# Kernel tuning notes

Hardware: AMD Instinct MI355X
Metric: run time of the kernel (lower is better)

The kernel has to match this reference:

```python
import jax, jax.numpy as jnp
import numpy as np

B, NB, F, N = 8192, 64, 256, 1_000_000
K = 8            # per-channel top-k
KS = K // 2 + 1  # conv1d kernel size = 5
H, OUT = 256, 128
DN = ('NWC', 'WIO', 'NWC')


def setup_inputs() -> dict:
    key = jax.random.key(0)
    ks = jax.random.split(key, 7)
    return {
        'node_ids': jax.random.randint(ks[0], (B,), 0, N, dtype=jnp.int64) if jax.config.jax_enable_x64 else jax.random.randint(ks[0], (B,), 0, N, dtype=jnp.int32),
        'neighbors': jax.random.randint(ks[1], (B, NB), 0, N, dtype=jnp.int32),
        'feat_table': jax.random.normal(ks[2], (N, F), dtype=jnp.float32),
        'W1': jax.random.normal(ks[3], (KS, F, H), dtype=jnp.float32) * 0.05,
        'b1': jnp.zeros((H,), dtype=jnp.float32),
        'W2': jax.random.normal(ks[4], (KS, H, OUT), dtype=jnp.float32) * 0.05,
        'b2': jnp.zeros((OUT,), dtype=jnp.float32),
    }


def reference(node_ids, neighbors, feat_table, W1, b1, W2, b2):
    node_feats = feat_table[node_ids][:, None, :]          # [B, 1, F]
    nb_feats = feat_table[neighbors]                       # [B, NB, F] irregular gather
    # per-channel top-k over neighbors
    topk, _ = jax.lax.top_k(jnp.transpose(nb_feats, (0, 2, 1)), K)  # [B, F, K]
    topk = jnp.transpose(topk, (0, 2, 1))                  # [B, K, F]
    x = jnp.concatenate([node_feats, topk], axis=1)        # [B, K+1, F]
    h = jax.lax.conv_general_dilated(x, W1, (1,), 'VALID', dimension_numbers=DN) + b1  # [B, K+2-KS, H]
    o = jax.lax.conv_general_dilated(h, W2, (1,), 'VALID', dimension_numbers=DN) + b2  # [B, 1, OUT]
    return o[:, 0, :]                                      # [B, OUT]
```

## Files before the change

### kernel.cpp

```cpp
#include <hip/hip_runtime.h>
#include <hip/hip_bf16.h>

namespace {
constexpr int kB    = 8192;
constexpr int kNB   = 64;
constexpr int kF    = 256;
constexpr int kK    = 8;
constexpr int kKS   = 5;
constexpr int kH    = 256;
constexpr int kOUT  = 128;
constexpr int kXR   = 9;
constexpr int kTO   = 5;
constexpr int kBM   = 16;

constexpr int XPAD = 258;
constexpr int HPAD = 1290;

constexpr size_t W1T_OFF = 0;
constexpr size_t W2T_OFF = W1T_OFF + (size_t)kKS * kH * kF * 2;

typedef __attribute__((ext_vector_type(8))) short short8;
typedef __attribute__((ext_vector_type(4))) float f32x4;
}

using bf16 = __hip_bfloat16;

__device__ __forceinline__ unsigned short f2bf(float f) {
  bf16 h = __float2bfloat16(f);
  return *reinterpret_cast<unsigned short*>(&h);
}

__global__ void convert_weights(const float* __restrict__ W1,
                                const float* __restrict__ W2,
                                bf16* __restrict__ w1t, bf16* __restrict__ w2t)
{
  const int i = blockIdx.x * 256 + threadIdx.x;
  const int stride = gridDim.x * 256;
  for (int idx = i; idx < kKS * kH * kF; idx += stride) {
    const int f  = idx & 255;
    const int hc = (idx >> 8) & 255;
    const int dt = idx >> 16;
    w1t[idx] = __float2bfloat16(W1[(dt * kF + f) * kH + hc]);
  }
  for (int idx = i; idx < kOUT * kKS * kH; idx += stride) {
    const int k = idx % (kKS * kH);
    const int o = idx / (kKS * kH);
    w2t[idx] = __float2bfloat16(W2[k * kOUT + o]);
  }
}

__global__ __launch_bounds__(256)
void fused_all(const int* __restrict__ node_ids,
               const int* __restrict__ neighbors,
               const float* __restrict__ feat,
               const bf16* __restrict__ w1t, const bf16* __restrict__ w2t,
               const float* __restrict__ b1, const float* __restrict__ b2,
               float* __restrict__ out)
{
  __shared__ bf16 smem[kBM * kXR * XPAD];
  bf16* xs = smem;
  bf16* hs = smem;

  const int tid  = threadIdx.x;
  const int wave = tid >> 6;
  const int lane = tid & 63;
  const int r = lane & 15;
  const int q = lane >> 4;
  const int bbase = blockIdx.x * kBM;
  const int f4 = lane << 2;

  for (int bb = 0; bb < 4; ++bb) {
    const int bl = wave * 4 + bb;
    const int b  = bbase + bl;
    const int myn = neighbors[(size_t)b * kNB + lane];
    const int nid = node_ids[b];
    const float4 nodev = *reinterpret_cast<const float4*>(feat + (size_t)nid * kF + f4);

    float tk[4][kK];
#pragma unroll
    for (int c = 0; c < 4; ++c)
#pragma unroll
      for (int k = 0; k < kK; ++k) tk[c][k] = -INFINITY;

    auto ce4 = [&](const float4& v) {
      const float vv[4] = {v.x, v.y, v.z, v.w};
#pragma unroll
      for (int c = 0; c < 4; ++c) {
        tk[c][kK - 1] = fmaxf(tk[c][kK - 1], vv[c]);
#pragma unroll
        for (int k = kK - 1; k > 0; --k) {
          const float hi = fmaxf(tk[c][k - 1], tk[c][k]);
          const float lo = fminf(tk[c][k - 1], tk[c][k]);
          tk[c][k - 1] = hi;
          tk[c][k]     = lo;
        }
      }
    };

    float4 buf[8];
#pragma unroll
    for (int i = 0; i < 8; ++i) {
      const int rr = __builtin_amdgcn_readlane(myn, i);
      buf[i] = *reinterpret_cast<const float4*>(feat + (size_t)rr * kF + f4);
    }
    for (int g = 1; g < 8; ++g) {
#pragma unroll
      for (int i = 0; i < 8; ++i) {
        const float4 v = buf[i];
        const int rr = __builtin_amdgcn_readlane(myn, g * 8 + i);
        buf[i] = *reinterpret_cast<const float4*>(feat + (size_t)rr * kF + f4);
        ce4(v);
      }
    }
#pragma unroll
    for (int i = 0; i < 8; ++i) ce4(buf[i]);

    bf16* xb = xs + (size_t)bl * kXR * XPAD + f4;
    {
      ushort4 s = {f2bf(nodev.x), f2bf(nodev.y), f2bf(nodev.z), f2bf(nodev.w)};
      *reinterpret_cast<ushort4*>(xb) = s;
    }
#pragma unroll
    for (int k = 0; k < kK; ++k) {
      ushort4 s = {f2bf(tk[0][k]), f2bf(tk[1][k]), f2bf(tk[2][k]), f2bf(tk[3][k])};
      *reinterpret_cast<ushort4*>(xb + (size_t)(1 + k) * XPAD) = s;
    }
  }
  __syncthreads();

  const int ntb = wave * 64;
  f32x4 acc[kTO][4];
#pragma unroll
  for (int n = 0; n < 4; ++n) {
    const float bv = b1[ntb + n * 16 + r];
#pragma unroll
    for (int m = 0; m < kTO; ++m) acc[m][n] = (f32x4){bv, bv, bv, bv};
  }

  for (int kk = 0; kk < 8; ++kk) {
    short8 a[kXR];
#pragma unroll
    for (int rr = 0; rr < kXR; ++rr)
      a[rr] = *reinterpret_cast<const short8*>(&xs[(r * kXR + rr) * XPAD + kk * 32 + q * 8]);
#pragma unroll
    for (int dt = 0; dt < kKS; ++dt) {
      short8 bfr[4];
#pragma unroll
      for (int n = 0; n < 4; ++n)
        bfr[n] = *reinterpret_cast<const short8*>(
            &w1t[((size_t)(dt * kH + ntb + n * 16 + r)) * kF + kk * 32 + q * 8]);
#pragma unroll
      for (int m = 0; m < kTO; ++m)
#pragma unroll
        for (int n = 0; n < 4; ++n)
          acc[m][n] = __builtin_amdgcn_mfma_f32_16x16x32_bf16(a[m + dt], bfr[n], acc[m][n], 0, 0, 0);
    }
  }
  __syncthreads();

#pragma unroll
  for (int m = 0; m < kTO; ++m)
#pragma unroll
    for (int n = 0; n < 4; ++n)
#pragma unroll
      for (int j = 0; j < 4; ++j)
        hs[(q * 4 + j) * HPAD + m * kH + ntb + n * 16 + r] = __float2bfloat16(acc[m][n][j]);
  __syncthreads();

  const int ob = wave * 32;
  f32x4 acc2[2];
#pragma unroll
  for (int n = 0; n < 2; ++n) {
    const float bv = b2[ob + n * 16 + r];
    acc2[n] = (f32x4){bv, bv, bv, bv};
  }
  for (int ks = 0; ks < 40; ++ks) {
    short8 a2 = *reinterpret_cast<const short8*>(&hs[r * HPAD + ks * 32 + q * 8]);
#pragma unroll
    for (int n = 0; n < 2; ++n) {
      short8 b2f = *reinterpret_cast<const short8*>(
          &w2t[(size_t)(ob + n * 16 + r) * (kKS * kH) + ks * 32 + q * 8]);
      acc2[n] = __builtin_amdgcn_mfma_f32_16x16x32_bf16(a2, b2f, acc2[n], 0, 0, 0);
    }
  }
#pragma unroll
  for (int n = 0; n < 2; ++n)
#pragma unroll
    for (int j = 0; j < 4; ++j)
      out[(size_t)(bbase + q * 4 + j) * kOUT + ob + n * 16 + r] = acc2[n][j];
}

extern "C" void kernel_launch(void* const* d_in, const int* in_sizes, int n_in,
                              void* d_out, int out_size, void* d_ws, size_t ws_size,
                              hipStream_t stream) {
  const int*   node_ids  = (const int*)  d_in[0];
  const int*   neighbors = (const int*)  d_in[1];
  const float* feat      = (const float*)d_in[2];
  const float* W1        = (const float*)d_in[3];
  const float* b1        = (const float*)d_in[4];
  const float* W2        = (const float*)d_in[5];
  const float* b2        = (const float*)d_in[6];
  float* out = (float*)d_out;

  char* ws = (char*)d_ws;
  bf16* w1t = (bf16*)(ws + W1T_OFF);
  bf16* w2t = (bf16*)(ws + W2T_OFF);

  convert_weights<<<512, 256, 0, stream>>>(W1, W2, w1t, w2t);
  fused_all<<<kB / kBM, 256, 0, stream>>>(node_ids, neighbors, feat, w1t, w2t, b1, b2, out);
}
```

Before: 139.1 us.

## Deepen gather prefetch, hoist per-row loads, use med3 top-k insertion

Moves the neighbor-index and node-feature loads for all four rows ahead of the top-k loop. Doubles the in-flight gather buffer from 8 to 16 float4 loads per lane to hide more latency on the random row gathers. Replaces the compare-exchange bubble insertion with a parallel fmed3-based sorted insertion, which cuts the ALU ops per insert. The larger buffer and full unrolling raise register pressure and may lower occupancy.

```diff
diff --git a/kernel.cpp b/kernel.cpp
--- a/kernel.cpp
+++ b/kernel.cpp
@@ -69,12 +69,19 @@
   const int bbase = blockIdx.x * kBM;
   const int f4 = lane << 2;
 
+  int   myn4[4];
+  float4 node4[4];
+#pragma unroll
   for (int bb = 0; bb < 4; ++bb) {
-    const int bl = wave * 4 + bb;
-    const int b  = bbase + bl;
-    const int myn = neighbors[(size_t)b * kNB + lane];
-    const int nid = node_ids[b];
-    const float4 nodev = *reinterpret_cast<const float4*>(feat + (size_t)nid * kF + f4);
+    const int b = bbase + wave * 4 + bb;
+    myn4[bb] = neighbors[(size_t)b * kNB + lane];
+    node4[bb] = *reinterpret_cast<const float4*>(feat + (size_t)node_ids[b] * kF + f4);
+  }
+
+#pragma unroll
+  for (int bb = 0; bb < 4; ++bb) {
+    const int bl  = wave * 4 + bb;
+    const int myn = myn4[bb];
 
     float tk[4][kK];
 #pragma unroll
@@ -82,42 +89,42 @@
 #pragma unroll
       for (int k = 0; k < kK; ++k) tk[c][k] = -INFINITY;
 
-    auto ce4 = [&](const float4& v) {
+    auto ins4 = [&](const float4& v) {
       const float vv[4] = {v.x, v.y, v.z, v.w};
 #pragma unroll
       for (int c = 0; c < 4; ++c) {
-        tk[c][kK - 1] = fmaxf(tk[c][kK - 1], vv[c]);
-#pragma unroll
-        for (int k = kK - 1; k > 0; --k) {
-          const float hi = fmaxf(tk[c][k - 1], tk[c][k]);
-          const float lo = fminf(tk[c][k - 1], tk[c][k]);
-          tk[c][k - 1] = hi;
-          tk[c][k]     = lo;
-        }
+        float nt[kK];
+        nt[0] = fmaxf(tk[c][0], vv[c]);
+#pragma unroll
+        for (int k = 1; k < kK; ++k)
+          nt[k] = __builtin_amdgcn_fmed3f(tk[c][k - 1], tk[c][k], vv[c]);
+#pragma unroll
+        for (int k = 0; k < kK; ++k) tk[c][k] = nt[k];
       }
     };
 
-    float4 buf[8];
-#pragma unroll
-    for (int i = 0; i < 8; ++i) {
+    float4 buf[16];
+#pragma unroll
+    for (int i = 0; i < 16; ++i) {
       const int rr = __builtin_amdgcn_readlane(myn, i);
       buf[i] = *reinterpret_cast<const float4*>(feat + (size_t)rr * kF + f4);
     }
-    for (int g = 1; g < 8; ++g) {
-#pragma unroll
-      for (int i = 0; i < 8; ++i) {
+#pragma unroll
+    for (int g = 1; g < 4; ++g) {
+#pragma unroll
+      for (int i = 0; i < 16; ++i) {
         const float4 v = buf[i];
-        const int rr = __builtin_amdgcn_readlane(myn, g * 8 + i);
+        const int rr = __builtin_amdgcn_readlane(myn, g * 16 + i);
         buf[i] = *reinterpret_cast<const float4*>(feat + (size_t)rr * kF + f4);
-        ce4(v);
+        ins4(v);
       }
     }
 #pragma unroll
-    for (int i = 0; i < 8; ++i) ce4(buf[i]);
+    for (int i = 0; i < 16; ++i) ins4(buf[i]);
 
     bf16* xb = xs + (size_t)bl * kXR * XPAD + f4;
     {
-      ushort4 s = {f2bf(nodev.x), f2bf(nodev.y), f2bf(nodev.z), f2bf(nodev.w)};
+      ushort4 s = {f2bf(node4[bb].x), f2bf(node4[bb].y), f2bf(node4[bb].z), f2bf(node4[bb].w)};
       *reinterpret_cast<ushort4*>(xb) = s;
     }
 #pragma unroll
```

Result: no change. 138.5 us (-0.4%).
